# Optimization experiments

Hardware: AMD Instinct MI355X
Metric: run time of the kernel (lower is better)

The kernel has to match this reference:

```python
import jax, jax.numpy as jnp
import numpy as np

DIM = 4096
N_HEADS = 32
N_KV_HEADS = 8
HEAD_DIM = DIM // N_HEADS          # 128
N_REPS = N_HEADS // N_KV_HEADS    # 4
MAX_SEQ = 2048
SEQ = 2048
BSZ = 1
ROPE_THETA = 500000.0
NEG_INF = -1e9


def _make_freqs():
    inv = 1.0 / (ROPE_THETA ** (np.arange(0, HEAD_DIM, 2, dtype=np.float32) / HEAD_DIM))
    t = np.arange(MAX_SEQ, dtype=np.float32)
    f = np.outer(t, inv)  # [MAX_SEQ, HEAD_DIM//2]
    return jnp.asarray(np.cos(f)), jnp.asarray(np.sin(f))


def setup_inputs() -> dict:
    key = jax.random.key(0)
    ks = jax.random.split(key, 6)
    scale = 1.0 / np.sqrt(DIM)
    x = jax.random.normal(ks[0], (BSZ, SEQ, DIM), dtype=jnp.float32)
    wq = jax.random.normal(ks[1], (N_HEADS * HEAD_DIM, DIM), dtype=jnp.float32) * scale
    wk = jax.random.normal(ks[2], (N_KV_HEADS * HEAD_DIM, DIM), dtype=jnp.float32) * scale
    wv = jax.random.normal(ks[3], (N_KV_HEADS * HEAD_DIM, DIM), dtype=jnp.float32) * scale
    wo = jax.random.normal(ks[4], (DIM, N_HEADS * HEAD_DIM), dtype=jnp.float32) * scale
    freqs_cos, freqs_sin = _make_freqs()
    freqs_cos, freqs_sin = freqs_cos[:SEQ], freqs_sin[:SEQ]
    # causal additive mask [SEQ, SEQ]
    mask = jnp.where(jnp.tril(jnp.ones((SEQ, SEQ), dtype=bool)), 0.0, NEG_INF).astype(jnp.float32)
    return {"x": x, "wq": wq, "wk": wk, "wv": wv, "wo": wo,
            "freqs_cos": freqs_cos, "freqs_sin": freqs_sin,
            "mask": mask, "start_pos": 0}


def _apply_rope(t, cos, sin):
    # t: [b, s, h, d]; cos/sin: [s, d//2]
    b, s, h, d = t.shape
    tr = t.reshape(b, s, h, d // 2, 2)
    re, im = tr[..., 0], tr[..., 1]
    c = cos[None, :, None, :]
    sn = sin[None, :, None, :]
    out = jnp.stack([re * c - im * sn, re * sn + im * c], axis=-1)
    return out.reshape(b, s, h, d)


def reference(x, wq, wk, wv, wo, freqs_cos, freqs_sin, mask, start_pos):
    b, s, _ = x.shape
    xq = (x @ wq.T).reshape(b, s, N_HEADS, HEAD_DIM)
    xk = (x @ wk.T).reshape(b, s, N_KV_HEADS, HEAD_DIM)
    xv = (x @ wv.T).reshape(b, s, N_KV_HEADS, HEAD_DIM)
    xq = _apply_rope(xq, freqs_cos, freqs_sin)
    xk = _apply_rope(xk, freqs_cos, freqs_sin)
    # KV cache write + read (start_pos is a static Python int)
    kv_len = start_pos + s
    k_cache = jnp.zeros((b, MAX_SEQ, N_KV_HEADS, HEAD_DIM), dtype=x.dtype)
    v_cache = jnp.zeros((b, MAX_SEQ, N_KV_HEADS, HEAD_DIM), dtype=x.dtype)
    k_cache = jax.lax.dynamic_update_slice(k_cache, xk, (0, start_pos, 0, 0))
    v_cache = jax.lax.dynamic_update_slice(v_cache, xv, (0, start_pos, 0, 0))
    keys = k_cache[:, :kv_len]   # [b, kv, Hkv, d]
    vals = v_cache[:, :kv_len]
    # GQA expand (repeat_interleave over kv heads)
    keys = jnp.broadcast_to(keys[:, :, :, None, :], (b, kv_len, N_KV_HEADS, N_REPS, HEAD_DIM)).reshape(b, kv_len, N_HEADS, HEAD_DIM)
    vals = jnp.broadcast_to(vals[:, :, :, None, :], (b, kv_len, N_KV_HEADS, N_REPS, HEAD_DIM)).reshape(b, kv_len, N_HEADS, HEAD_DIM)
    scores = jnp.einsum('bqhd,bkhd->bhqk', xq, keys) / jnp.sqrt(jnp.float32(HEAD_DIM))
    scores = scores + mask[None, None, :, :]
    probs = jax.nn.softmax(scores.astype(jnp.float32), axis=-1).astype(xq.dtype)
    out = jnp.einsum('bhqk,bkhd->bqhd', probs, vals).reshape(b, s, N_HEADS * HEAD_DIM)
    return out @ wo.T
```

## Files before the change

### kernel.cpp

```cpp
#include <hip/hip_runtime.h>

#define SEQ   2048
#define DIM   4096
#define NH    32
#define NKV   8
#define HD    128
#define KVDIM 1024

typedef __attribute__((ext_vector_type(8))) short bf16x8;
typedef __attribute__((ext_vector_type(4))) float f32x4;

static __device__ __forceinline__ unsigned short f2bf(float x) {
    unsigned int u = __float_as_uint(x);
    unsigned int r = (u + 0x7fffu + ((u >> 16) & 1u)) >> 16;
    return (unsigned short)r;
}

__global__ __launch_bounds__(256) void cvt_kernel(const float* __restrict__ s,
                                                  unsigned short* __restrict__ d, int n4)
{
    int i = blockIdx.x * 256 + threadIdx.x;
    int stride = gridDim.x * 256;
    for (; i < n4; i += stride) {
        float4 v = reinterpret_cast<const float4*>(s)[i];
        ushort4 u;
        u.x = f2bf(v.x); u.y = f2bf(v.y); u.z = f2bf(v.z); u.w = f2bf(v.w);
        reinterpret_cast<ushort4*>(d)[i] = u;
    }
}

template<bool ABF, bool WBF, int MODE>
__global__ __launch_bounds__(256) void gemm_bt(
    const void* __restrict__ Ap, const void* __restrict__ Wp,
    void* __restrict__ Cp, void* __restrict__ Cp2, void* __restrict__ Cp3, int ldC,
    const float* __restrict__ cosT, const float* __restrict__ sinT)
{
    constexpr int AS = ABF ? 32 : 40;
    constexpr int BS = WBF ? 32 : 40;
    __shared__ unsigned short As[128 * AS];
    __shared__ unsigned short Bs[128 * BS];

    const int t  = threadIdx.x;
    const int w  = t >> 6, l = t & 63;
    const int lr = l & 15, lg = l >> 4;
    const int wm = (w >> 1) * 64, wn = (w & 1) * 64;
    const int m0 = blockIdx.y * 128, n0 = blockIdx.x * 128;

    f32x4 acc[4][4] = {};

    for (int k0 = 0; k0 < 4096; k0 += 32) {
        if constexpr (ABF) {
            const unsigned short* A = (const unsigned short*)Ap;
            #pragma unroll
            for (int i = 0; i < 2; ++i) {
                const unsigned short* src =
                    A + (size_t)(m0 + i * 64 + w * 16 + (l >> 2)) * 4096 + k0 + (l & 3) * 8;
                __builtin_amdgcn_global_load_lds(
                    (const __attribute__((address_space(1))) void*)src,
                    (__attribute__((address_space(3))) void*)&As[(i * 64 + w * 16) * 32],
                    16, 0, 0);
            }
        } else {
            const float* A = (const float*)Ap;
            #pragma unroll
            for (int i = 0; i < 4; ++i) {
                int row = (t >> 3) + 32 * i, kc = (t & 7) * 4;
                float4 v = *reinterpret_cast<const float4*>(A + (size_t)(m0 + row) * 4096 + k0 + kc);
                ushort4 u;
                u.x = f2bf(v.x); u.y = f2bf(v.y); u.z = f2bf(v.z); u.w = f2bf(v.w);
                *reinterpret_cast<ushort4*>(&As[row * 40 + kc]) = u;
            }
        }
        if constexpr (WBF) {
            const unsigned short* B = (const unsigned short*)Wp;
            #pragma unroll
            for (int i = 0; i < 2; ++i) {
                const unsigned short* src =
                    B + (size_t)(n0 + i * 64 + w * 16 + (l >> 2)) * 4096 + k0 + (l & 3) * 8;
                __builtin_amdgcn_global_load_lds(
                    (const __attribute__((address_space(1))) void*)src,
                    (__attribute__((address_space(3))) void*)&Bs[(i * 64 + w * 16) * 32],
                    16, 0, 0);
            }
        } else {
            const float* B = (const float*)Wp;
            #pragma unroll
            for (int i = 0; i < 4; ++i) {
                int row = (t >> 3) + 32 * i, kc = (t & 7) * 4;
                float4 v = *reinterpret_cast<const float4*>(B + (size_t)(n0 + row) * 4096 + k0 + kc);
                ushort4 u;
                u.x = f2bf(v.x); u.y = f2bf(v.y); u.z = f2bf(v.z); u.w = f2bf(v.w);
                *reinterpret_cast<ushort4*>(&Bs[row * 40 + kc]) = u;
            }
        }
        __syncthreads();

        bf16x8 af[4], bfr[4];
        #pragma unroll
        for (int m = 0; m < 4; ++m)
            af[m] = *reinterpret_cast<const bf16x8*>(&As[(wm + m * 16 + lr) * AS + lg * 8]);
        #pragma unroll
        for (int n = 0; n < 4; ++n)
            bfr[n] = *reinterpret_cast<const bf16x8*>(&Bs[(wn + n * 16 + lr) * BS + lg * 8]);
        #pragma unroll
        for (int m = 0; m < 4; ++m)
            #pragma unroll
            for (int n = 0; n < 4; ++n)
                acc[m][n] = __builtin_amdgcn_mfma_f32_16x16x32_bf16(af[m], bfr[n], acc[m][n], 0, 0, 0);
        __syncthreads();
    }

    if constexpr (MODE == 3) {
        float* C = (float*)Cp;
        #pragma unroll
        for (int m = 0; m < 4; ++m)
            #pragma unroll
            for (int n = 0; n < 4; ++n)
                #pragma unroll
                for (int j = 0; j < 4; ++j)
                    C[(size_t)(m0 + wm + m * 16 + lg * 4 + j) * ldC + n0 + wn + n * 16 + lr] =
                        acc[m][n][j];
    } else if constexpr (MODE == 2) {
        unsigned short* VT = (unsigned short*)Cp;
        #pragma unroll
        for (int m = 0; m < 4; ++m)
            #pragma unroll
            for (int n = 0; n < 4; ++n) {
                int col = n0 + wn + n * 16 + lr;
                int r0  = m0 + wm + m * 16 + lg * 4;
                ushort4 u;
                u.x = f2bf(acc[m][n][0]); u.y = f2bf(acc[m][n][1]);
                u.z = f2bf(acc[m][n][2]); u.w = f2bf(acc[m][n][3]);
                *reinterpret_cast<ushort4*>(&VT[(size_t)col * SEQ + r0]) = u;
            }
    } else if constexpr (MODE == 1) {
        unsigned short* C = (unsigned short*)Cp;
        #pragma unroll
        for (int m = 0; m < 4; ++m)
            #pragma unroll
            for (int n = 0; n < 4; ++n) {
                int col = n0 + wn + n * 16 + lr;
                int p   = (col & 127) >> 1;
                float sg = (col & 1) ? 1.f : -1.f;
                #pragma unroll
                for (int j = 0; j < 4; ++j) {
                    int row = m0 + wm + m * 16 + lg * 4 + j;
                    float v  = acc[m][n][j];
                    float pr = __shfl_xor(v, 1);
                    float o  = v * cosT[row * 64 + p] + sg * sinT[row * 64 + p] * pr;
                    C[(size_t)row * ldC + col] = f2bf(o);
                }
            }
    } else {
        if (n0 < 5120) {
            unsigned short* C;
            int ldc2, csub;
            if (n0 < 4096) { C = (unsigned short*)Cp;  ldc2 = DIM;   csub = 0;    }
            else           { C = (unsigned short*)Cp2; ldc2 = KVDIM; csub = 4096; }
            #pragma unroll
            for (int m = 0; m < 4; ++m)
                #pragma unroll
                for (int n = 0; n < 4; ++n) {
                    int col = n0 + wn + n * 16 + lr - csub;
                    int p   = (col & 127) >> 1;
                    float sg = (col & 1) ? 1.f : -1.f;
                    #pragma unroll
                    for (int j = 0; j < 4; ++j) {
                        int row = m0 + wm + m * 16 + lg * 4 + j;
                        float v  = acc[m][n][j];
                        float pr = __shfl_xor(v, 1);
                        float o  = v * cosT[row * 64 + p] + sg * sinT[row * 64 + p] * pr;
                        C[(size_t)row * ldc2 + col] = f2bf(o);
                    }
                }
        } else {
            unsigned short* VT = (unsigned short*)Cp3;
            #pragma unroll
            for (int m = 0; m < 4; ++m)
                #pragma unroll
                for (int n = 0; n < 4; ++n) {
                    int col = n0 + wn + n * 16 + lr - 5120;
                    int r0  = m0 + wm + m * 16 + lg * 4;
                    ushort4 u;
                    u.x = f2bf(acc[m][n][0]); u.y = f2bf(acc[m][n][1]);
                    u.z = f2bf(acc[m][n][2]); u.w = f2bf(acc[m][n][3]);
                    *reinterpret_cast<ushort4*>(&VT[(size_t)col * SEQ + r0]) = u;
                }
        }
    }
}

__global__ __launch_bounds__(512, 4) void attn_kernel(const unsigned short* __restrict__ Qb,
                                                      const unsigned short* __restrict__ Kb,
                                                      const unsigned short* __restrict__ Vt,
                                                      unsigned short* __restrict__ Ob)
{
    __shared__ unsigned short Kl[2][64 * 128];
    __shared__ unsigned short Vl[2][128 * 64];
    __shared__ unsigned short Pl[8][16 * 64];

    const int t  = threadIdx.x;
    const int w  = t >> 6, l = t & 63;
    const int lr = l & 15, lg = l >> 4;
    const int qb = (gridDim.x - 1) - blockIdx.x;
    const int h  = blockIdx.y;
    const int kvh = h >> 2;
    const int qw = qb * 128 + w * 16;

    bf16x8 qf[4];
    #pragma unroll
    for (int f = 0; f < 4; ++f)
        qf[f] = *reinterpret_cast<const bf16x8*>(Qb + (size_t)(qw + lr) * DIM + h * HD + f * 32 + lg * 8);

    f32x4 po[8] = {};
    float lsum[4] = {0.f, 0.f, 0.f, 0.f};
    const float scale = 0.08838834764831845f;
    const int nt = 2 * qb + 2;

    auto STAGE = [&](int kt, int b) {
        const int kbase = kt * 64;
        #pragma unroll
        for (int i = 0; i < 2; ++i) {
            int key = w * 8 + 4 * i + (l >> 4);
            const unsigned short* src = Kb + (size_t)(kbase + key) * KVDIM + kvh * HD
                                           + (((l & 15) ^ (key & 7)) << 3);
            __builtin_amdgcn_global_load_lds(
                (const __attribute__((address_space(1))) void*)src,
                (__attribute__((address_space(3))) void*)&Kl[b][(w * 8 + 4 * i) * 128],
                16, 0, 0);
        }
        #pragma unroll
        for (int i = 0; i < 2; ++i) {
            int d = w * 16 + 8 * i + (l >> 3);
            const unsigned short* src = Vt + (size_t)(kvh * HD + d) * SEQ + kbase
                                           + (((l & 7) ^ (d & 7)) << 3);
            __builtin_amdgcn_global_load_lds(
                (const __attribute__((address_space(1))) void*)src,
                (__attribute__((address_space(3))) void*)&Vl[b][(w * 16 + 8 * i) * 64],
                16, 0, 0);
        }
    };

    STAGE(0, 0);
    __syncthreads();
    int cur = 0;

    for (int kt = 0; kt < nt; ++kt) {
        const int kbase = kt * 64;
        if (kt + 1 < nt) STAGE(kt + 1, cur ^ 1);

        if (kbase <= qw + 15) {
            f32x4 sc[4] = {};
            #pragma unroll
            for (int c = 0; c < 4; ++c) {
                int key = c * 16 + lr;
                #pragma unroll
                for (int f = 0; f < 4; ++f) {
                    bf16x8 kb = *reinterpret_cast<const bf16x8*>(
                        &Kl[cur][(key * 128 + f * 32 + lg * 8) ^ ((key & 7) << 3)]);
                    sc[c] = __builtin_amdgcn_mfma_f32_16x16x32_bf16(qf[f], kb, sc[c], 0, 0, 0);
                }
            }

            const bool diag = (kbase + 63 > qw);
            #pragma unroll
            for (int j = 0; j < 4; ++j) {
                int q = qw + lg * 4 + j;
                int prow = lg * 4 + j;
                float ps = 0.f;
                #pragma unroll
                for (int c = 0; c < 4; ++c) {
                    float p = __expf(sc[c][j] * scale - 8.0f);
                    if (diag && (kbase + c * 16 + lr > q)) p = 0.f;
                    ps += p;
                    Pl[w][(prow * 64 + c * 16 + lr) ^ ((prow & 7) << 3)] = f2bf(p);
                }
                lsum[j] += ps;
            }

            bf16x8 pa0 = *reinterpret_cast<const bf16x8*>(
                &Pl[w][(lr * 64 + lg * 8) ^ ((lr & 7) << 3)]);
            bf16x8 pa1 = *reinterpret_cast<const bf16x8*>(
                &Pl[w][(lr * 64 + 32 + lg * 8) ^ ((lr & 7) << 3)]);
            #pragma unroll
            for (int o = 0; o < 8; ++o) {
                int d = o * 16 + lr;
                bf16x8 bv0 = *reinterpret_cast<const bf16x8*>(
                    &Vl[cur][(d * 64 + lg * 8) ^ ((d & 7) << 3)]);
                bf16x8 bv1 = *reinterpret_cast<const bf16x8*>(
                    &Vl[cur][(d * 64 + 32 + lg * 8) ^ ((d & 7) << 3)]);
                po[o] = __builtin_amdgcn_mfma_f32_16x16x32_bf16(pa0, bv0, po[o], 0, 0, 0);
                po[o] = __builtin_amdgcn_mfma_f32_16x16x32_bf16(pa1, bv1, po[o], 0, 0, 0);
            }
        }
        __syncthreads();
        cur ^= 1;
    }

    #pragma unroll
    for (int j = 0; j < 4; ++j) {
        float s = lsum[j];
        s += __shfl_xor(s, 1);
        s += __shfl_xor(s, 2);
        s += __shfl_xor(s, 4);
        s += __shfl_xor(s, 8);
        float inv = 1.f / s;
        int q = qw + lg * 4 + j;
        #pragma unroll
        for (int o = 0; o < 8; ++o)
            Ob[(size_t)q * DIM + h * HD + o * 16 + lr] = f2bf(po[o][j] * inv);
    }
}

extern "C" void kernel_launch(void* const* d_in, const int* in_sizes, int n_in,
                              void* d_out, int out_size, void* d_ws, size_t ws_size,
                              hipStream_t stream) {
    const float* x    = (const float*)d_in[0];
    const float* wq   = (const float*)d_in[1];
    const float* wk   = (const float*)d_in[2];
    const float* wv   = (const float*)d_in[3];
    const float* wo   = (const float*)d_in[4];
    const float* cosT = (const float*)d_in[5];
    const float* sinT = (const float*)d_in[6];
    float* out = (float*)d_out;

    unsigned short* ws = (unsigned short*)d_ws;
    const bool big = ws_size >= (size_t)136 * 1024 * 1024;

    if (big) {
        unsigned short* xb   = ws;
        unsigned short* wqkv = xb   + (size_t)SEQ * DIM;
        unsigned short* wob  = wqkv + (size_t)(DIM + 2 * KVDIM) * DIM;
        unsigned short* Qb   = wob  + (size_t)DIM * DIM;
        unsigned short* Kb   = Qb   + (size_t)SEQ * DIM;
        unsigned short* Vtb  = Kb   + (size_t)SEQ * KVDIM;
        unsigned short* Ob   = Vtb  + (size_t)KVDIM * SEQ;

        cvt_kernel<<<2048, 256, 0, stream>>>(x,  xb,   SEQ * DIM / 4);
        cvt_kernel<<<2048, 256, 0, stream>>>(wq, wqkv, DIM * DIM / 4);
        cvt_kernel<<<2048, 256, 0, stream>>>(wk, wqkv + (size_t)DIM * DIM, KVDIM * DIM / 4);
        cvt_kernel<<<2048, 256, 0, stream>>>(wv, wqkv + (size_t)(DIM + KVDIM) * DIM, KVDIM * DIM / 4);
        cvt_kernel<<<2048, 256, 0, stream>>>(wo, wob,  DIM * DIM / 4);

        gemm_bt<true, true, 5><<<dim3(48, 16), 256, 0, stream>>>(
            xb, wqkv, Qb, Kb, Vtb, 0, cosT, sinT);
        attn_kernel<<<dim3(16, 32), 512, 0, stream>>>(Qb, Kb, Vtb, Ob);
        gemm_bt<true, true, 3><<<dim3(32, 16), 256, 0, stream>>>(
            Ob, wob, out, nullptr, nullptr, DIM, nullptr, nullptr);
    } else {
        unsigned short* Qb  = ws;
        unsigned short* Kb  = Qb  + (size_t)SEQ * DIM;
        unsigned short* Vtb = Kb  + (size_t)SEQ * KVDIM;
        unsigned short* Ob  = Vtb + (size_t)KVDIM * SEQ;

        gemm_bt<false, false, 1><<<dim3(32, 16), 256, 0, stream>>>(
            x, wq, Qb, nullptr, nullptr, DIM, cosT, sinT);
        gemm_bt<false, false, 1><<<dim3(8, 16),  256, 0, stream>>>(
            x, wk, Kb, nullptr, nullptr, KVDIM, cosT, sinT);
        gemm_bt<false, false, 2><<<dim3(8, 16),  256, 0, stream>>>(
            x, wv, Vtb, nullptr, nullptr, 0, nullptr, nullptr);
        attn_kernel<<<dim3(16, 32), 512, 0, stream>>>(Qb, Kb, Vtb, Ob);
        gemm_bt<true, false, 3><<<dim3(32, 16), 256, 0, stream>>>(
            Ob, wo, out, nullptr, nullptr, DIM, nullptr, nullptr);
    }
}
```

Measured before the change: 625.8 us.

## Double-buffer bf16 GEMM LDS tiles, swizzle workgroup order, fuse conversion kernels

The all-bf16 GEMM path now uses two LDS buffers, so the async global-to-LDS load of the next K tile is issued while MFMAs run on the current tile. This removes one barrier per iteration and hides load latency. Workgroup IDs are remapped in groups of 8, which changes which tiles run at the same time and is aimed at cache locality. The five separate fp32-to-bf16 conversion launches are merged into one kernel that writes the contiguous workspace. In exchange, LDS use doubles and the conversion loop gains per-element branching.

```diff
diff --git a/kernel.cpp b/kernel.cpp
--- a/kernel.cpp
+++ b/kernel.cpp
@@ -14,6 +14,36 @@
     unsigned int u = __float_as_uint(x);
     unsigned int r = (u + 0x7fffu + ((u >> 16) & 1u)) >> 16;
     return (unsigned short)r;
+}
+
+#define N_X4   2097152
+#define B0_4   2097152
+#define B1_4   6291456
+#define B2_4   7340032
+#define B3_4   8388608
+#define TOT4  12582912
+
+__global__ __launch_bounds__(256) void cvt5_kernel(const float* __restrict__ x,
+                                                   const float* __restrict__ wq,
+                                                   const float* __restrict__ wk,
+                                                   const float* __restrict__ wv,
+                                                   const float* __restrict__ wo,
+                                                   unsigned short* __restrict__ d)
+{
+    int i = blockIdx.x * 256 + threadIdx.x;
+    const int stride = gridDim.x * 256;
+    for (; i < TOT4; i += stride) {
+        const float* s; int off;
+        if      (i < B0_4) { s = x;  off = i;         }
+        else if (i < B1_4) { s = wq; off = i - B0_4;  }
+        else if (i < B2_4) { s = wk; off = i - B1_4;  }
+        else if (i < B3_4) { s = wv; off = i - B2_4;  }
+        else               { s = wo; off = i - B3_4;  }
+        float4 v = reinterpret_cast<const float4*>(s)[off];
+        ushort4 u;
+        u.x = f2bf(v.x); u.y = f2bf(v.y); u.z = f2bf(v.z); u.w = f2bf(v.w);
+        reinterpret_cast<ushort4*>(d)[i] = u;
+    }
 }
 
 __global__ __launch_bounds__(256) void cvt_kernel(const float* __restrict__ s,
@@ -35,79 +65,111 @@
     void* __restrict__ Cp, void* __restrict__ Cp2, void* __restrict__ Cp3, int ldC,
     const float* __restrict__ cosT, const float* __restrict__ sinT)
 {
+    constexpr bool DB = ABF && WBF;
     constexpr int AS = ABF ? 32 : 40;
     constexpr int BS = WBF ? 32 : 40;
-    __shared__ unsigned short As[128 * AS];
-    __shared__ unsigned short Bs[128 * BS];
+    __shared__ unsigned short As[DB ? 2 : 1][128 * AS];
+    __shared__ unsigned short Bs[DB ? 2 : 1][128 * BS];
 
     const int t  = threadIdx.x;
     const int w  = t >> 6, l = t & 63;
     const int lr = l & 15, lg = l >> 4;
     const int wm = (w >> 1) * 64, wn = (w & 1) * 64;
-    const int m0 = blockIdx.y * 128, n0 = blockIdx.x * 128;
+
+    const int gx  = gridDim.x;
+    const int nwg = gx * gridDim.y;
+    int flat = blockIdx.y * gx + blockIdx.x;
+    if ((nwg & 7) == 0) flat = (flat & 7) * (nwg >> 3) + (flat >> 3);
+    const int m0 = (flat / gx) * 128, n0 = (flat % gx) * 128;
 
     f32x4 acc[4][4] = {};
 
-    for (int k0 = 0; k0 < 4096; k0 += 32) {
-        if constexpr (ABF) {
-            const unsigned short* A = (const unsigned short*)Ap;
+    if constexpr (DB) {
+        const unsigned short* A = (const unsigned short*)Ap;
+        const unsigned short* B = (const unsigned short*)Wp;
+
+        auto STAGE = [&](int k0, int b) {
             #pragma unroll
             for (int i = 0; i < 2; ++i) {
                 const unsigned short* src =
                     A + (size_t)(m0 + i * 64 + w * 16 + (l >> 2)) * 4096 + k0 + (l & 3) * 8;
                 __builtin_amdgcn_global_load_lds(
                     (const __attribute__((address_space(1))) void*)src,
-                    (__attribute__((address_space(3))) void*)&As[(i * 64 + w * 16) * 32],
+                    (__attribute__((address_space(3))) void*)&As[b][(i * 64 + w * 16) * 32],
                     16, 0, 0);
             }
-        } else {
-            const float* A = (const float*)Ap;
-            #pragma unroll
-            for (int i = 0; i < 4; ++i) {
-                int row = (t >> 3) + 32 * i, kc = (t & 7) * 4;
-                float4 v = *reinterpret_cast<const float4*>(A + (size_t)(m0 + row) * 4096 + k0 + kc);
-                ushort4 u;
-                u.x = f2bf(v.x); u.y = f2bf(v.y); u.z = f2bf(v.z); u.w = f2bf(v.w);
-                *reinterpret_cast<ushort4*>(&As[row * 40 + kc]) = u;
-            }
-        }
-        if constexpr (WBF) {
-            const unsigned short* B = (const unsigned short*)Wp;
             #pragma unroll
             for (int i = 0; i < 2; ++i) {
                 const unsigned short* src =
                     B + (size_t)(n0 + i * 64 + w * 16 + (l >> 2)) * 4096 + k0 + (l & 3) * 8;
                 __builtin_amdgcn_global_load_lds(
                     (const __attribute__((address_space(1))) void*)src,
-                    (__attribute__((address_space(3))) void*)&Bs[(i * 64 + w * 16) * 32],
+                    (__attribute__((address_space(3))) void*)&Bs[b][(i * 64 + w * 16) * 32],
                     16, 0, 0);
             }
-        } else {
-            const float* B = (const float*)Wp;
-            #pragma unroll
-            for (int i = 0; i < 4; ++i) {
-                int row = (t >> 3) + 32 * i, kc = (t & 7) * 4;
-                float4 v = *reinterpret_cast<const float4*>(B + (size_t)(n0 + row) * 4096 + k0 + kc);
-                ushort4 u;
-                u.x = f2bf(v.x); u.y = f2bf(v.y); u.z = f2bf(v.z); u.w = f2bf(v.w);
-                *reinterpret_cast<ushort4*>(&Bs[row * 40 + kc]) = u;
-            }
-        }
+        };
+
+        STAGE(0, 0);
         __syncthreads();
-
-        bf16x8 af[4], bfr[4];
-        #pragma unroll
-        for (int m = 0; m < 4; ++m)
-            af[m] = *reinterpret_cast<const bf16x8*>(&As[(wm + m * 16 + lr) * AS + lg * 8]);
-        #pragma unroll
-        for (int n = 0; n < 4; ++n)
-            bfr[n] = *reinterpret_cast<const bf16x8*>(&Bs[(wn + n * 16 + lr) * BS + lg * 8]);
-        #pragma unroll
-        for (int m = 0; m < 4; ++m)
+        int cur = 0;
+        for (int k0 = 0; k0 < 4096; k0 += 32) {
+            if (k0 + 32 < 4096) STAGE(k0 + 32, cur ^ 1);
+
+            bf16x8 af[4], bfr[4];
+            #pragma unroll
+            for (int m = 0; m < 4; ++m)
+                af[m] = *reinterpret_cast<const bf16x8*>(&As[cur][(wm + m * 16 + lr) * 32 + lg * 8]);
             #pragma unroll
             for (int n = 0; n < 4; ++n)
-                acc[m][n] = __builtin_amdgcn_mfma_f32_16x16x32_bf16(af[m], bfr[n], acc[m][n], 0, 0, 0);
-        __syncthreads();
+                bfr[n] = *reinterpret_cast<const bf16x8*>(&Bs[cur][(wn + n * 16 + lr) * 32 + lg * 8]);
+            #pragma unroll
+            for (int m = 0; m < 4; ++m)
+                #pragma unroll
+                for (int n = 0; n < 4; ++n)
+                    acc[m][n] = __builtin_amdgcn_mfma_f32_16x16x32_bf16(af[m], bfr[n], acc[m][n], 0, 0, 0);
+            __syncthreads();
+            cur ^= 1;
+        }
+    } else {
+        for (int k0 = 0; k0 < 4096; k0 += 32) {
+            {
+                const float* A = (const float*)Ap;
+                #pragma unroll
+                for (int i = 0; i < 4; ++i) {
+                    int row = (t >> 3) + 32 * i, kc = (t & 7) * 4;
+                    float4 v = *reinterpret_cast<const float4*>(A + (size_t)(m0 + row) * 4096 + k0 + kc);
+                    ushort4 u;
+                    u.x = f2bf(v.x); u.y = f2bf(v.y); u.z = f2bf(v.z); u.w = f2bf(v.w);
+                    *reinterpret_cast<ushort4*>(&As[0][row * 40 + kc]) = u;
+                }
+            }
+            {
+                const float* B = (const float*)Wp;
+                #pragma unroll
+                for (int i = 0; i < 4; ++i) {
+                    int row = (t >> 3) + 32 * i, kc = (t & 7) * 4;
+                    float4 v = *reinterpret_cast<const float4*>(B + (size_t)(n0 + row) * 4096 + k0 + kc);
+                    ushort4 u;
+                    u.x = f2bf(v.x); u.y = f2bf(v.y); u.z = f2bf(v.z); u.w = f2bf(v.w);
+                    *reinterpret_cast<ushort4*>(&Bs[0][row * 40 + kc]) = u;
+                }
+            }
+            __syncthreads();
+
+            bf16x8 af[4], bfr[4];
+            #pragma unroll
+            for (int m = 0; m < 4; ++m)
+                af[m] = *reinterpret_cast<const bf16x8*>(&As[0][(wm + m * 16 + lr) * AS + lg * 8]);
+            #pragma unroll
+            for (int n = 0; n < 4; ++n)
+                bfr[n] = *reinterpret_cast<const bf16x8*>(&Bs[0][(wn + n * 16 + lr) * BS + lg * 8]);
+            #pragma unroll
+            for (int m = 0; m < 4; ++m)
+                #pragma unroll
+                for (int n = 0; n < 4; ++n)
+                    acc[m][n] = __builtin_amdgcn_mfma_f32_16x16x32_bf16(af[m], bfr[n], acc[m][n], 0, 0, 0);
+            __syncthreads();
+        }
     }
 
     if constexpr (MODE == 3) {
@@ -336,11 +398,7 @@
         unsigned short* Vtb  = Kb   + (size_t)SEQ * KVDIM;
         unsigned short* Ob   = Vtb  + (size_t)KVDIM * SEQ;
 
-        cvt_kernel<<<2048, 256, 0, stream>>>(x,  xb,   SEQ * DIM / 4);
-        cvt_kernel<<<2048, 256, 0, stream>>>(wq, wqkv, DIM * DIM / 4);
-        cvt_kernel<<<2048, 256, 0, stream>>>(wk, wqkv + (size_t)DIM * DIM, KVDIM * DIM / 4);
-        cvt_kernel<<<2048, 256, 0, stream>>>(wv, wqkv + (size_t)(DIM + KVDIM) * DIM, KVDIM * DIM / 4);
-        cvt_kernel<<<2048, 256, 0, stream>>>(wo, wob,  DIM * DIM / 4);
+        cvt5_kernel<<<2048, 256, 0, stream>>>(x, wq, wk, wv, wo, ws);
 
         gemm_bt<true, true, 5><<<dim3(48, 16), 256, 0, stream>>>(
             xb, wqkv, Qb, Kb, Vtb, 0, cosT, sinT);
```

After: 638.4 us. 1.02x slower.
